# Kernel optimization log

Measured on AMD Instinct MI355X. Metric: run time of the kernel, lower is better.

Reference implementation:

```python
import jax, jax.numpy as jnp
import numpy as np


def setup_inputs() -> dict:
    key = jax.random.key(0)
    ks = jax.random.split(key, 8)
    B, C, H, W = 4, 256, 56, 56
    Cq = C // 8
    s = 0.05  # small init scale for conv weights, like kaiming-ish for 1x1 convs
    return {
        "x": jax.random.normal(ks[0], (B, C, H, W), jnp.float32),
        "Wq": jax.random.normal(ks[1], (Cq, C), jnp.float32) * s,
        "bq": jax.random.normal(ks[2], (Cq,), jnp.float32) * s,
        "Wk": jax.random.normal(ks[3], (Cq, C), jnp.float32) * s,
        "bk": jax.random.normal(ks[4], (Cq,), jnp.float32) * s,
        "Wv": jax.random.normal(ks[5], (C, C), jnp.float32) * s,
        "bv": jax.random.normal(ks[6], (C,), jnp.float32) * s,
        "gamma": jax.random.normal(ks[7], (1,), jnp.float32),
    }


def reference(x, Wq, bq, Wk, bk, Wv, bv, gamma):
    B, C, H, W = x.shape
    N = H * W
    xf = x.reshape(B, C, N)  # flatten spatial

    # 1x1 convs == channel matmuls
    q = jnp.einsum('oc,bcn->bon', Wq, xf) + bq[None, :, None]   # [B,Cq,N]
    k = jnp.einsum('oc,bcn->bon', Wk, xf) + bk[None, :, None]   # [B,Cq,N]
    v = jnp.einsum('oc,bcn->bon', Wv, xf) + bv[None, :, None]   # [B,C,N]

    # lipschitz_norm from weights: u=||Q||_F, v=max row-norm of K^T, w=max row-norm of V^T
    u = jnp.linalg.norm(Wq)
    vn = jnp.max(jnp.linalg.norm(Wk.T, axis=1))
    wn = jnp.max(jnp.linalg.norm(Wv.T, axis=1))
    norm_value = jnp.maximum(u * vn, u * wn)  # maximum(u*v, v*u, u*w)

    # energy[b,i,j] = <q[:,i], k[:,j]>, scaled by custom Lipschitz norm
    energy = jnp.einsum('bci,bcj->bij', q, k) / norm_value      # [B,N,N]
    attention = jax.nn.softmax(energy, axis=-1)

    # out[b,c,i] = sum_j v[b,c,j] * attention[b,i,j]
    out = jnp.einsum('bcj,bij->bci', v, attention).reshape(B, C, H, W)

    # lipschitz_bound: exp(sqrt(3)) * sqrt(N/C) + 2*sqrt(6)
    bound = np.float32(np.exp(np.sqrt(3.0)) * np.sqrt(N / C) + 2.0 * np.sqrt(6.0))
    out = out / bound

    return gamma * out + x
```

## Files before the change

### kernel.cpp

```cpp
#include <hip/hip_runtime.h>

#define N_SP 3136
#define C_CH 256
#define CQ   32
#define NB   4
#define JT   64
#define NJT  49
#define QT   64
#define INV_BOUND 0.04051569f
#define LOG2E 1.44269504f

typedef __attribute__((ext_vector_type(8))) short bf16x8;
typedef __attribute__((ext_vector_type(4))) float f32x4;
typedef __attribute__((ext_vector_type(2))) long long l64x2;
typedef unsigned short u16;
typedef unsigned int   u32;
typedef unsigned char  u8;
typedef long long      l64;

#define MFMA16(a,b,c) __builtin_amdgcn_mfma_f32_16x16x32_bf16(a,b,c,0,0,0)
#define MFMA8(a,b,c)  __builtin_amdgcn_mfma_f32_16x16x32_bf8_fp8(a,b,c,0,0,0)

__device__ __forceinline__ u16 f2b(float f) {
    u32 u = __builtin_bit_cast(u32, f);
    u += 0x7fffu + ((u >> 16) & 1u);
    return (u16)(u >> 16);
}
__device__ __forceinline__ u8 f2fp8(float f) {
    return (u8)(__builtin_amdgcn_cvt_pk_fp8_f32(f, f, 0, false) & 0xff);
}
__device__ __forceinline__ void dma16(const void* g, void* l) {
    __builtin_amdgcn_global_load_lds((const __attribute__((address_space(1))) u32*)g,
                                     (__attribute__((address_space(3))) u32*)l, 16, 0, 0);
}
__device__ __forceinline__ void dma4(const void* g, void* l) {
    __builtin_amdgcn_global_load_lds((const __attribute__((address_space(1))) u32*)g,
                                     (__attribute__((address_space(3))) u32*)l, 4, 0, 0);
}

__global__ __launch_bounds__(256) void stage1_kernel(
    const float* __restrict__ x, const float* __restrict__ Wq,
    const float* __restrict__ Wk, const float* __restrict__ Wv,
    u8* __restrict__ xT, u8* __restrict__ Wqb, u8* __restrict__ Wkb,
    u8* __restrict__ Wvb, float* __restrict__ scale_out,
    float* __restrict__ kmax)
{
    __shared__ float smem[64 * 65];
    const int t = threadIdx.x;
    const int bid = blockIdx.x;

    if (bid < 784) {
        float (*tile)[65] = (float(*)[65])smem;
        const int ct = bid & 3, nt = (bid >> 2) % 49, b = bid / 196;
        const int c0 = ct * 64, n0 = nt * 64;
        const int cc = t >> 4, nn4 = (t & 15) * 4;
        #pragma unroll
        for (int k = 0; k < 4; ++k) {
            int cl = cc + k * 16;
            float4 v = *(const float4*)(x + (size_t)(b * C_CH + c0 + cl) * N_SP + n0 + nn4);
            tile[cl][nn4] = v.x; tile[cl][nn4 + 1] = v.y;
            tile[cl][nn4 + 2] = v.z; tile[cl][nn4 + 3] = v.w;
        }
        __syncthreads();
        const int c4 = (t & 15) * 4, nn = t >> 4;
        #pragma unroll
        for (int k = 0; k < 4; ++k) {
            int nl = nn + k * 16;
            ushort4 o;
            o.x = f2b(tile[c4 + 0][nl]); o.y = f2b(tile[c4 + 1][nl]);
            o.z = f2b(tile[c4 + 2][nl]); o.w = f2b(tile[c4 + 3][nl]);
            const int off = ((c0 + c4) * 2) ^ ((nl & 15) << 5);
            *(ushort4*)(xT + (size_t)(b * N_SP + n0 + nl) * 512 + off) = o;
        }
    } else if (bid < 864) {
        int idx = (bid - 784) * 256 + t;
        const float* src; u8* dst; int off;
        if (idx < 2048)      { src = Wq; dst = Wqb; off = idx; }
        else if (idx < 4096) { src = Wk; dst = Wkb; off = idx - 2048; }
        else                 { src = Wv; dst = Wvb; off = idx - 4096; }
        float4 v = *(const float4*)(src + off * 4);
        ushort4 o; o.x = f2b(v.x); o.y = f2b(v.y); o.z = f2b(v.z); o.w = f2b(v.w);
        const int row = off >> 6, inner = (off & 63) * 8;
        *(ushort4*)(dst + row * 512 + (inner ^ ((row & 15) << 5))) = o;
    } else {
        if (t < NB) kmax[t] = 0.f;
        float* red = smem;
        float u2 = 0.f;
        for (int i = t; i < CQ * C_CH; i += 256) { float w = Wq[i]; u2 += w * w; }
        red[t] = u2; __syncthreads();
        #pragma unroll
        for (int s = 128; s > 0; s >>= 1) { if (t < s) red[t] += red[t + s]; __syncthreads(); }
        float u2t = red[0]; __syncthreads();
        float vn2 = 0.f;
        for (int o = 0; o < CQ; ++o)   { float w = Wk[o * C_CH + t]; vn2 += w * w; }
        float wn2 = 0.f;
        for (int o = 0; o < C_CH; ++o) { float w = Wv[o * C_CH + t]; wn2 += w * w; }
        red[t] = fmaxf(vn2, wn2); __syncthreads();
        #pragma unroll
        for (int s = 128; s > 0; s >>= 1) { if (t < s) red[t] = fmaxf(red[t], red[t + s]); __syncthreads(); }
        if (t == 0) scale_out[0] = 1.0f / (sqrtf(u2t) * sqrtf(red[0]));
    }
}

__global__ __launch_bounds__(256) void qkv_mfma(
    const u8* __restrict__ xT, const u8* __restrict__ Wqb,
    const u8* __restrict__ Wkb, const u8* __restrict__ Wvb,
    const float* __restrict__ bq, const float* __restrict__ bk,
    const float* __restrict__ bv, const float* __restrict__ scale_p,
    u16* __restrict__ qT, u8* __restrict__ Kg, u8* __restrict__ Vg,
    float* __restrict__ qnorm, float* __restrict__ kmax)
{
    __shared__ __align__(16) u8 xTl[32768];
    __shared__ __align__(16) u8 Wl[32768];

    const int t = threadIdx.x;
    const int split = blockIdx.x / 196, tile = blockIdx.x % 196;
    const int b = tile / 49, nt = tile % 49;
    const int w = t >> 6, lane = t & 63, li = t & 15, g = (t >> 4) & 3;
    const int n = nt * 64 + w * 16 + li;
    const int r0 = (split - 1) * 64;
    const f32x4 zero = {0.f, 0.f, 0.f, 0.f};

    {
        const u8* xsrc = xT + (size_t)(b * N_SP + nt * 64) * 512;
        #pragma unroll
        for (int i = 0; i < 8; ++i)
            dma16(xsrc + w * 8192 + i * 1024 + lane * 16, xTl + w * 8192 + i * 1024);
        if (split == 0) {
            #pragma unroll
            for (int i = 0; i < 4; ++i)
                dma16(Wqb + w * 4096 + i * 1024 + lane * 16, Wl + w * 4096 + i * 1024);
            #pragma unroll
            for (int i = 0; i < 4; ++i)
                dma16(Wkb + w * 4096 + i * 1024 + lane * 16, Wl + 16384 + w * 4096 + i * 1024);
        } else {
            const u8* wsrc = Wvb + (size_t)r0 * 512;
            #pragma unroll
            for (int i = 0; i < 8; ++i)
                dma16(wsrc + w * 8192 + i * 1024 + lane * 16, Wl + w * 8192 + i * 1024);
        }
    }
    asm volatile("s_waitcnt vmcnt(0)" ::: "memory");
    __syncthreads();

    const int swz = li << 5;
    bf16x8 xf[8];
    #pragma unroll
    for (int ks = 0; ks < 8; ++ks)
        xf[ks] = *(const bf16x8*)(xTl + (w * 16 + li) * 512 + ((ks * 64 + 16 * g) ^ swz));

    if (split == 0) {
        f32x4 aq0 = zero, aq1 = zero, ak0 = zero, ak1 = zero;
        #pragma unroll
        for (int ks = 0; ks < 8; ++ks) {
            const int o = (ks * 64 + 16 * g) ^ swz;
            bf16x8 w0 = *(const bf16x8*)(Wl + li * 512 + o);
            bf16x8 w1 = *(const bf16x8*)(Wl + (16 + li) * 512 + o);
            bf16x8 w2 = *(const bf16x8*)(Wl + 16384 + li * 512 + o);
            bf16x8 w3 = *(const bf16x8*)(Wl + 16384 + (16 + li) * 512 + o);
            aq0 = MFMA16(w0, xf[ks], aq0);
            aq1 = MFMA16(w1, xf[ks], aq1);
            ak0 = MFMA16(w2, xf[ks], ak0);
            ak1 = MFMA16(w3, xf[ks], ak1);
        }
        const float scf = scale_p[0] * LOG2E;
        f32x4 bq0 = *(const f32x4*)(bq + 4 * g);
        f32x4 bq1 = *(const f32x4*)(bq + 16 + 4 * g);
        f32x4 bk0 = *(const f32x4*)(bk + 4 * g);
        f32x4 bk1 = *(const f32x4*)(bk + 16 + 4 * g);
        float qn2 = 0.f, kn2 = 0.f;
        ushort4 s0, s1;
        #pragma unroll
        for (int r = 0; r < 4; ++r) {
            float q0 = (aq0[r] + bq0[r]) * scf;
            float q1 = (aq1[r] + bq1[r]) * scf;
            qn2 += q0 * q0 + q1 * q1;
            ((u16*)&s0)[r] = f2b(q0); ((u16*)&s1)[r] = f2b(q1);
        }
        *(ushort4*)(qT + (size_t)(b * N_SP + n) * CQ + 4 * g)      = s0;
        *(ushort4*)(qT + (size_t)(b * N_SP + n) * CQ + 16 + 4 * g) = s1;
        #pragma unroll
        for (int r = 0; r < 4; ++r) {
            float k0 = ak0[r] + bk0[r];
            float k1 = ak1[r] + bk1[r];
            kn2 += k0 * k0 + k1 * k1;
            ((u16*)&s0)[r] = f2b(k0); ((u16*)&s1)[r] = f2b(k1);
        }
        u8* krow = Kg + ((size_t)b * N_SP + n) * 64;
        const int swn = ((n >> 1) & 3) << 4;
        *(ushort4*)(krow + ((8 * g) ^ swn))      = s0;
        *(ushort4*)(krow + ((32 + 8 * g) ^ swn)) = s1;

        qn2 += __shfl_xor(qn2, 16); qn2 += __shfl_xor(qn2, 32);
        kn2 += __shfl_xor(kn2, 16); kn2 += __shfl_xor(kn2, 32);
        if (g == 0) qnorm[b * N_SP + n] = sqrtf(qn2);
        float kn = sqrtf(kn2);
        #pragma unroll
        for (int d = 1; d < 16; d <<= 1) kn = fmaxf(kn, __shfl_xor(kn, d));
        if ((t & 63) == 0) atomicMax((int*)(kmax + b), __float_as_int(kn));
    } else {
        f32x4 a[4] = {zero, zero, zero, zero};
        #pragma unroll
        for (int ks = 0; ks < 8; ++ks) {
            const int o = (ks * 64 + 16 * g) ^ swz;
            #pragma unroll
            for (int fr = 0; fr < 4; ++fr) {
                bf16x8 wf = *(const bf16x8*)(Wl + (fr * 16 + li) * 512 + o);
                a[fr] = MFMA16(wf, xf[ks], a[fr]);
            }
        }
        const int jj = w * 16 + li;
        const int p = ((jj >> 5) & 1) * 8 + ((jj >> 3) & 3) * 16 + (jj & 7);
        u8* vtile = Vg + (size_t)(b * NJT + nt) * 16384;
        #pragma unroll
        for (int fr = 0; fr < 4; ++fr) {
            f32x4 bb = *(const f32x4*)(bv + r0 + fr * 16 + 4 * g);
            #pragma unroll
            for (int r = 0; r < 4; ++r) {
                const int c = r0 + fr * 16 + 4 * g + r;
                vtile[c * 64 + (p ^ (((c >> 1) & 3) << 4))] = f2fp8(a[fr][r] + bb[r]);
            }
        }
    }
}

__global__ __launch_bounds__(512) void attn_mfma(
    const u16* __restrict__ qT, const u8* __restrict__ Kg,
    const u8* __restrict__ Vg, const float* __restrict__ x,
    const float* __restrict__ gamma_p, const float* __restrict__ qnorm,
    const float* __restrict__ kmax, float* __restrict__ out)
{
    __shared__ __align__(16) u8 smem[86016];
    u8* const Vl = smem;
    u8* const Kl = smem + 65536;
    u8* const Pl = smem + 81920;

    const int t = threadIdx.x;
    const int w = t >> 6, li = t & 15, g = (t >> 4) & 3;
    const int jh = w & 3, qh = w >> 2;
    const int cw = w * 32;
    const int swz = ((li >> 1) & 3) << 4;

    const int b  = blockIdx.x / NJT;
    const int i0 = (blockIdx.x % NJT) * QT;

    const u16* qTb = qT + (size_t)b * N_SP * CQ;
    const u8*  Kbb = Kg + (size_t)b * N_SP * 64;
    const u8*  Vbb = Vg + (size_t)b * NJT * 16384;
    const float kmb = kmax[b];
    const f32x4 zero = {0.f, 0.f, 0.f, 0.f};

    const int qA = 2 * qh, qB = 2 * qh + 1;
    const bf16x8 qfA = *(const bf16x8*)(qTb + (size_t)(i0 + qA * 16 + li) * CQ + 8 * g);
    const bf16x8 qfB = *(const bf16x8*)(qTb + (size_t)(i0 + qB * 16 + li) * CQ + 8 * g);
    const float mrA = qnorm[b * N_SP + i0 + qA * 16 + li] * kmb;
    const float mrB = qnorm[b * N_SP + i0 + qB * 16 + li] * kmb;

    f32x4 acc[4][2];
    #pragma unroll
    for (int qq = 0; qq < 4; ++qq) { acc[qq][0] = zero; acc[qq][1] = zero; }
    float lsA = 0.f, lsB = 0.f;

    #define ISSUE(jt_, s_) do {                                               \
        const u8* vsrc_ = Vbb + (size_t)(jt_) * 16384;                        \
        const u8* ksrc_ = Kbb + (size_t)(jt_) * 4096;                         \
        _Pragma("unroll")                                                     \
        for (int i_ = 0; i_ < 2; ++i_)                                        \
            dma16(vsrc_ + i_ * 8192 + t * 16,                                 \
                  Vl + (s_) * 16384 + i_ * 8192 + w * 1024);                  \
        _Pragma("unroll")                                                     \
        for (int i_ = 0; i_ < 2; ++i_)                                        \
            dma4(ksrc_ + i_ * 2048 + t * 4,                                   \
                 Kl + (s_) * 4096 + i_ * 2048 + w * 256);                     \
    } while (0)

    ISSUE(0, 0);
    ISSUE(1, 1);
    ISSUE(2, 2);

    const int p0 = ((jh >> 1) & 1) * 8 + ((jh * 2 + (g >> 1)) & 3) * 16 + 4 * (g & 1);

    for (int it = 0; it < NJT; ++it) {
        const int cur = it & 3;
        asm volatile("s_waitcnt vmcnt(8) lgkmcnt(0)" ::: "memory");
        __builtin_amdgcn_s_barrier();
        asm volatile("" ::: "memory");

        {
            int jn = it + 3; if (jn > NJT - 1) jn = NJT - 1;
            ISSUE(jn, (cur + 3) & 3);
        }

        const u8* Kc = Kl + cur * 4096;
        bf16x8 kf = *(const bf16x8*)(Kc + (jh * 16 + li) * 64 + ((16 * g) ^ swz));
        f32x4 sA = MFMA16(kf, qfA, zero);
        f32x4 sB = MFMA16(kf, qfB, zero);
        {
            float a0 = exp2f(sA[0] - mrA), a1 = exp2f(sA[1] - mrA);
            float a2 = exp2f(sA[2] - mrA), a3 = exp2f(sA[3] - mrA);
            lsA += (a0 + a1) + (a2 + a3);
            int pk = __builtin_amdgcn_cvt_pk_bf8_f32(a0, a1, 0, false);
            pk = __builtin_amdgcn_cvt_pk_bf8_f32(a2, a3, pk, true);
            *(u32*)(Pl + (qA * 16 + li) * 64 + (p0 ^ swz)) = (u32)pk;
            float b0 = exp2f(sB[0] - mrB), b1 = exp2f(sB[1] - mrB);
            float b2 = exp2f(sB[2] - mrB), b3 = exp2f(sB[3] - mrB);
            lsB += (b0 + b1) + (b2 + b3);
            pk = __builtin_amdgcn_cvt_pk_bf8_f32(b0, b1, 0, false);
            pk = __builtin_amdgcn_cvt_pk_bf8_f32(b2, b3, pk, true);
            *(u32*)(Pl + (qB * 16 + li) * 64 + (p0 ^ swz)) = (u32)pk;
        }
        asm volatile("s_waitcnt lgkmcnt(0)" ::: "memory");
        __builtin_amdgcn_s_barrier();
        asm volatile("" ::: "memory");

        const u8* Vc = Vl + cur * 16384;
        __builtin_amdgcn_s_setprio(1);
        l64x2 pa0 = *(const l64x2*)(Pl + (0 * 16 + li) * 64 + ((16 * g) ^ swz));
        l64x2 pa1 = *(const l64x2*)(Pl + (1 * 16 + li) * 64 + ((16 * g) ^ swz));
        l64x2 pa2 = *(const l64x2*)(Pl + (2 * 16 + li) * 64 + ((16 * g) ^ swz));
        l64x2 pa3 = *(const l64x2*)(Pl + (3 * 16 + li) * 64 + ((16 * g) ^ swz));
        l64x2 v0  = *(const l64x2*)(Vc + (cw + li) * 64 + ((16 * g) ^ swz));
        l64x2 v1  = *(const l64x2*)(Vc + (cw + 16 + li) * 64 + ((16 * g) ^ swz));
        acc[0][0] = MFMA8(pa0[0], v0[0], acc[0][0]);
        acc[0][1] = MFMA8(pa0[0], v1[0], acc[0][1]);
        acc[1][0] = MFMA8(pa1[0], v0[0], acc[1][0]);
        acc[1][1] = MFMA8(pa1[0], v1[0], acc[1][1]);
        acc[2][0] = MFMA8(pa2[0], v0[0], acc[2][0]);
        acc[2][1] = MFMA8(pa2[0], v1[0], acc[2][1]);
        acc[3][0] = MFMA8(pa3[0], v0[0], acc[3][0]);
        acc[3][1] = MFMA8(pa3[0], v1[0], acc[3][1]);
        acc[0][0] = MFMA8(pa0[1], v0[1], acc[0][0]);
        acc[0][1] = MFMA8(pa0[1], v1[1], acc[0][1]);
        acc[1][0] = MFMA8(pa1[1], v0[1], acc[1][0]);
        acc[1][1] = MFMA8(pa1[1], v1[1], acc[1][1]);
        acc[2][0] = MFMA8(pa2[1], v0[1], acc[2][0]);
        acc[2][1] = MFMA8(pa2[1], v1[1], acc[2][1]);
        acc[3][0] = MFMA8(pa3[1], v0[1], acc[3][0]);
        acc[3][1] = MFMA8(pa3[1], v1[1], acc[3][1]);
        __builtin_amdgcn_s_setprio(0);
    }
    #undef ISSUE

    lsA += __shfl_xor(lsA, 16); lsA += __shfl_xor(lsA, 32);
    lsB += __shfl_xor(lsB, 16); lsB += __shfl_xor(lsB, 32);
    __syncthreads();
    float* red       = (float*)Pl;
    float* red_final = (float*)(Pl + 1024);
    if ((t & 63) < 16) {
        red[w * 32 + li]      = lsA;
        red[w * 32 + 16 + li] = lsB;
    }
    __syncthreads();
    if (t < 64) {
        const int h = t >> 4, l2 = t & 15;
        float s = 0.f;
        #pragma unroll
        for (int jw = 0; jw < 4; ++jw)
            s += red[((h >> 1) * 4 + jw) * 32 + (h & 1) * 16 + l2];
        red_final[t] = s;
    }
    __syncthreads();

    const float gsc = gamma_p[0] * INV_BOUND;
    #pragma unroll
    for (int qq = 0; qq < 4; ++qq) {
        f32x4 lsv = *(const f32x4*)(red_final + qq * 16 + 4 * g);
        f32x4 rinv;
        #pragma unroll
        for (int r = 0; r < 4; ++r) rinv[r] = gsc / lsv[r];
        #pragma unroll
        for (int cf = 0; cf < 2; ++cf) {
            const int c = cw + cf * 16 + li;
            const size_t base = ((size_t)b * C_CH + c) * N_SP + i0 + qq * 16 + 4 * g;
            float4 xv = *(const float4*)(x + base);
            float4 o;
            o.x = acc[qq][cf][0] * rinv[0] + xv.x;
            o.y = acc[qq][cf][1] * rinv[1] + xv.y;
            o.z = acc[qq][cf][2] * rinv[2] + xv.z;
            o.w = acc[qq][cf][3] * rinv[3] + xv.w;
            *(float4*)(out + base) = o;
        }
    }
}

extern "C" void kernel_launch(void* const* d_in, const int* in_sizes, int n_in,
                              void* d_out, int out_size, void* d_ws, size_t ws_size,
                              hipStream_t stream)
{
    const float* x  = (const float*)d_in[0];
    const float* Wq = (const float*)d_in[1];
    const float* bq = (const float*)d_in[2];
    const float* Wk = (const float*)d_in[3];
    const float* bk = (const float*)d_in[4];
    const float* Wv = (const float*)d_in[5];
    const float* bv = (const float*)d_in[6];
    const float* gm = (const float*)d_in[7];
    float* out = (float*)d_out;
    float* ws  = (float*)d_ws;

    float* scale = ws;
    float* kmax  = ws + 4;
    float* qnorm = ws + 8;
    u8* Wqb = (u8*)(ws + 8 + NB * N_SP);
    u8* Wkb = Wqb + 32 * 512;
    u8* Wvb = Wkb + 32 * 512;
    u8* xT  = Wvb + 256 * 512;
    u16* qT = (u16*)(xT + (size_t)NB * N_SP * 512);
    u8* Kg  = (u8*)(qT + (size_t)NB * N_SP * CQ);
    u8* Vg  = Kg + (size_t)NB * N_SP * 64;

    stage1_kernel<<<865, 256, 0, stream>>>(x, Wq, Wk, Wv, xT, Wqb, Wkb, Wvb, scale, kmax);
    qkv_mfma<<<980, 256, 0, stream>>>(xT, Wqb, Wkb, Wvb, bq, bk, bv, scale, qT, Kg, Vg, qnorm, kmax);
    attn_mfma<<<NB * NJT, 512, 0, stream>>>(qT, Kg, Vg, x, gm, qnorm, kmax, out);
}
```

Before: 87.92 us.

## Split attention key range across two blocks with larger query tiles and combine pass

Doubles the query tile to 128 rows and splits the 49 key tiles into two halves handled by separate blocks, giving 200 blocks instead of 196. Each block writes its unnormalized bf16 numerator and row sums to the workspace, and a new combine kernel adds the two halves, normalizes, scales by gamma and adds the residual. The aim is to reuse each streamed K/V tile across more query rows, halving K/V traffic per query, while keeping the grid filled through the key split. The cost is an extra kernel launch, a partial-result round-trip through memory, bf16 rounding of the partial numerators, and more accumulator registers, which may lower occupancy.

```diff
diff --git a/kernel.cpp b/kernel.cpp
--- a/kernel.cpp
+++ b/kernel.cpp
@@ -6,7 +6,9 @@
 #define NB   4
 #define JT   64
 #define NJT  49
-#define QT   64
+#define QT   128
+#define NQT  25
+#define JSPL 2
 #define INV_BOUND 0.04051569f
 #define LOG2E 1.44269504f
 
@@ -25,6 +27,9 @@
     u32 u = __builtin_bit_cast(u32, f);
     u += 0x7fffu + ((u >> 16) & 1u);
     return (u16)(u >> 16);
+}
+__device__ __forceinline__ float b2f(u16 v) {
+    return __builtin_bit_cast(float, (u32)v << 16);
 }
 __device__ __forceinline__ u8 f2fp8(float f) {
     return (u8)(__builtin_amdgcn_cvt_pk_fp8_f32(f, f, 0, false) & 0xff);
@@ -226,11 +231,11 @@
 
 __global__ __launch_bounds__(512) void attn_mfma(
     const u16* __restrict__ qT, const u8* __restrict__ Kg,
-    const u8* __restrict__ Vg, const float* __restrict__ x,
-    const float* __restrict__ gamma_p, const float* __restrict__ qnorm,
-    const float* __restrict__ kmax, float* __restrict__ out)
+    const u8* __restrict__ Vg, const float* __restrict__ qnorm,
+    const float* __restrict__ kmax, u16* __restrict__ numP,
+    float* __restrict__ lsP)
 {
-    __shared__ __align__(16) u8 smem[86016];
+    __shared__ __align__(16) u8 smem[88064];
     u8* const Vl = smem;
     u8* const Kl = smem + 65536;
     u8* const Pl = smem + 81920;
@@ -241,8 +246,12 @@
     const int cw = w * 32;
     const int swz = ((li >> 1) & 3) << 4;
 
-    const int b  = blockIdx.x / NJT;
-    const int i0 = (blockIdx.x % NJT) * QT;
+    const int bid = blockIdx.x;
+    const int b = bid / 50, rem = bid % 50;
+    const int qt = rem >> 1, js = rem & 1;
+    const int i0 = qt * QT;
+    const int jbeg = js ? 25 : 0, jend = js ? 49 : 25;
+    const int nIter = jend - jbeg;
 
     const u16* qTb = qT + (size_t)b * N_SP * CQ;
     const u8*  Kbb = Kg + (size_t)b * N_SP * 64;
@@ -250,16 +259,19 @@
     const float kmb = kmax[b];
     const f32x4 zero = {0.f, 0.f, 0.f, 0.f};
 
-    const int qA = 2 * qh, qB = 2 * qh + 1;
-    const bf16x8 qfA = *(const bf16x8*)(qTb + (size_t)(i0 + qA * 16 + li) * CQ + 8 * g);
-    const bf16x8 qfB = *(const bf16x8*)(qTb + (size_t)(i0 + qB * 16 + li) * CQ + 8 * g);
-    const float mrA = qnorm[b * N_SP + i0 + qA * 16 + li] * kmb;
-    const float mrB = qnorm[b * N_SP + i0 + qB * 16 + li] * kmb;
-
-    f32x4 acc[4][2];
+    bf16x8 qf[4]; float mr[4];
     #pragma unroll
-    for (int qq = 0; qq < 4; ++qq) { acc[qq][0] = zero; acc[qq][1] = zero; }
-    float lsA = 0.f, lsB = 0.f;
+    for (int f = 0; f < 4; ++f) {
+        int qr = i0 + (qh * 4 + f) * 16 + li;
+        qr = qr < N_SP ? qr : N_SP - 1;
+        qf[f] = *(const bf16x8*)(qTb + (size_t)qr * CQ + 8 * g);
+        mr[f] = qnorm[b * N_SP + qr] * kmb;
+    }
+
+    f32x4 acc[8][2];
+    #pragma unroll
+    for (int qq = 0; qq < 8; ++qq) { acc[qq][0] = zero; acc[qq][1] = zero; }
+    float ls4[4] = {0.f, 0.f, 0.f, 0.f};
 
     #define ISSUE(jt_, s_) do {                                               \
         const u8* vsrc_ = Vbb + (size_t)(jt_) * 16384;                        \
@@ -274,40 +286,35 @@
                  Kl + (s_) * 4096 + i_ * 2048 + w * 256);                     \
     } while (0)
 
-    ISSUE(0, 0);
-    ISSUE(1, 1);
-    ISSUE(2, 2);
+    ISSUE(jbeg, 0);
+    ISSUE(jbeg + 1, 1);
+    ISSUE(jbeg + 2, 2);
 
     const int p0 = ((jh >> 1) & 1) * 8 + ((jh * 2 + (g >> 1)) & 3) * 16 + 4 * (g & 1);
 
-    for (int it = 0; it < NJT; ++it) {
-        const int cur = it & 3;
+    for (int ii = 0; ii < nIter; ++ii) {
+        const int it = jbeg + ii;
+        const int cur = ii & 3;
         asm volatile("s_waitcnt vmcnt(8) lgkmcnt(0)" ::: "memory");
         __builtin_amdgcn_s_barrier();
         asm volatile("" ::: "memory");
 
         {
-            int jn = it + 3; if (jn > NJT - 1) jn = NJT - 1;
+            int jn = it + 3; if (jn > jend - 1) jn = jend - 1;
             ISSUE(jn, (cur + 3) & 3);
         }
 
         const u8* Kc = Kl + cur * 4096;
         bf16x8 kf = *(const bf16x8*)(Kc + (jh * 16 + li) * 64 + ((16 * g) ^ swz));
-        f32x4 sA = MFMA16(kf, qfA, zero);
-        f32x4 sB = MFMA16(kf, qfB, zero);
-        {
-            float a0 = exp2f(sA[0] - mrA), a1 = exp2f(sA[1] - mrA);
-            float a2 = exp2f(sA[2] - mrA), a3 = exp2f(sA[3] - mrA);
-            lsA += (a0 + a1) + (a2 + a3);
+        #pragma unroll
+        for (int f = 0; f < 4; ++f) {
+            f32x4 s = MFMA16(kf, qf[f], zero);
+            float a0 = exp2f(s[0] - mr[f]), a1 = exp2f(s[1] - mr[f]);
+            float a2 = exp2f(s[2] - mr[f]), a3 = exp2f(s[3] - mr[f]);
+            ls4[f] += (a0 + a1) + (a2 + a3);
             int pk = __builtin_amdgcn_cvt_pk_bf8_f32(a0, a1, 0, false);
             pk = __builtin_amdgcn_cvt_pk_bf8_f32(a2, a3, pk, true);
-            *(u32*)(Pl + (qA * 16 + li) * 64 + (p0 ^ swz)) = (u32)pk;
-            float b0 = exp2f(sB[0] - mrB), b1 = exp2f(sB[1] - mrB);
-            float b2 = exp2f(sB[2] - mrB), b3 = exp2f(sB[3] - mrB);
-            lsB += (b0 + b1) + (b2 + b3);
-            pk = __builtin_amdgcn_cvt_pk_bf8_f32(b0, b1, 0, false);
-            pk = __builtin_amdgcn_cvt_pk_bf8_f32(b2, b3, pk, true);
-            *(u32*)(Pl + (qB * 16 + li) * 64 + (p0 ^ swz)) = (u32)pk;
+            *(u32*)(Pl + ((qh * 4 + f) * 16 + li) * 64 + (p0 ^ swz)) = (u32)pk;
         }
         asm volatile("s_waitcnt lgkmcnt(0)" ::: "memory");
         __builtin_amdgcn_s_barrier();
@@ -315,71 +322,82 @@
 
         const u8* Vc = Vl + cur * 16384;
         __builtin_amdgcn_s_setprio(1);
-        l64x2 pa0 = *(const l64x2*)(Pl + (0 * 16 + li) * 64 + ((16 * g) ^ swz));
-        l64x2 pa1 = *(const l64x2*)(Pl + (1 * 16 + li) * 64 + ((16 * g) ^ swz));
-        l64x2 pa2 = *(const l64x2*)(Pl + (2 * 16 + li) * 64 + ((16 * g) ^ swz));
-        l64x2 pa3 = *(const l64x2*)(Pl + (3 * 16 + li) * 64 + ((16 * g) ^ swz));
-        l64x2 v0  = *(const l64x2*)(Vc + (cw + li) * 64 + ((16 * g) ^ swz));
-        l64x2 v1  = *(const l64x2*)(Vc + (cw + 16 + li) * 64 + ((16 * g) ^ swz));
-        acc[0][0] = MFMA8(pa0[0], v0[0], acc[0][0]);
-        acc[0][1] = MFMA8(pa0[0], v1[0], acc[0][1]);
-        acc[1][0] = MFMA8(pa1[0], v0[0], acc[1][0]);
-        acc[1][1] = MFMA8(pa1[0], v1[0], acc[1][1]);
-        acc[2][0] = MFMA8(pa2[0], v0[0], acc[2][0]);
-        acc[2][1] = MFMA8(pa2[0], v1[0], acc[2][1]);
-        acc[3][0] = MFMA8(pa3[0], v0[0], acc[3][0]);
-        acc[3][1] = MFMA8(pa3[0], v1[0], acc[3][1]);
-        acc[0][0] = MFMA8(pa0[1], v0[1], acc[0][0]);
-        acc[0][1] = MFMA8(pa0[1], v1[1], acc[0][1]);
-        acc[1][0] = MFMA8(pa1[1], v0[1], acc[1][0]);
-        acc[1][1] = MFMA8(pa1[1], v1[1], acc[1][1]);
-        acc[2][0] = MFMA8(pa2[1], v0[1], acc[2][0]);
-        acc[2][1] = MFMA8(pa2[1], v1[1], acc[2][1]);
-        acc[3][0] = MFMA8(pa3[1], v0[1], acc[3][0]);
-        acc[3][1] = MFMA8(pa3[1], v1[1], acc[3][1]);
+        l64x2 v0 = *(const l64x2*)(Vc + (cw + li) * 64 + ((16 * g) ^ swz));
+        l64x2 v1 = *(const l64x2*)(Vc + (cw + 16 + li) * 64 + ((16 * g) ^ swz));
+        #pragma unroll
+        for (int qq = 0; qq < 8; ++qq) {
+            l64x2 pa = *(const l64x2*)(Pl + (qq * 16 + li) * 64 + ((16 * g) ^ swz));
+            acc[qq][0] = MFMA8(pa[0], v0[0], acc[qq][0]);
+            acc[qq][1] = MFMA8(pa[0], v1[0], acc[qq][1]);
+            acc[qq][0] = MFMA8(pa[1], v0[1], acc[qq][0]);
+            acc[qq][1] = MFMA8(pa[1], v1[1], acc[qq][1]);
+        }
         __builtin_amdgcn_s_setprio(0);
     }
     #undef ISSUE
 
-    lsA += __shfl_xor(lsA, 16); lsA += __shfl_xor(lsA, 32);
-    lsB += __shfl_xor(lsB, 16); lsB += __shfl_xor(lsB, 32);
+    #pragma unroll
+    for (int f = 0; f < 4; ++f) {
+        ls4[f] += __shfl_xor(ls4[f], 16);
+        ls4[f] += __shfl_xor(ls4[f], 32);
+    }
     __syncthreads();
-    float* red       = (float*)Pl;
-    float* red_final = (float*)(Pl + 1024);
+    float* red = (float*)Pl;
     if ((t & 63) < 16) {
-        red[w * 32 + li]      = lsA;
-        red[w * 32 + 16 + li] = lsB;
+        #pragma unroll
+        for (int f = 0; f < 4; ++f) red[w * 64 + f * 16 + li] = ls4[f];
     }
     __syncthreads();
-    if (t < 64) {
-        const int h = t >> 4, l2 = t & 15;
-        float s = 0.f;
-        #pragma unroll
-        for (int jw = 0; jw < 4; ++jw)
-            s += red[((h >> 1) * 4 + jw) * 32 + (h & 1) * 16 + l2];
-        red_final[t] = s;
-    }
-    __syncthreads();
-
-    const float gsc = gamma_p[0] * INV_BOUND;
+    if (t < QT) {
+        const int qh2 = t >> 6, rowin = t & 63;
+        float s = red[(qh2 * 4 + 0) * 64 + rowin] + red[(qh2 * 4 + 1) * 64 + rowin]
+                + red[(qh2 * 4 + 2) * 64 + rowin] + red[(qh2 * 4 + 3) * 64 + rowin];
+        lsP[(size_t)bid * QT + t] = s;
+    }
+
+    u16* np = numP + (size_t)bid * QT * C_CH;
     #pragma unroll
-    for (int qq = 0; qq < 4; ++qq) {
-        f32x4 lsv = *(const f32x4*)(red_final + qq * 16 + 4 * g);
-        f32x4 rinv;
-        #pragma unroll
-        for (int r = 0; r < 4; ++r) rinv[r] = gsc / lsv[r];
+    for (int qq = 0; qq < 8; ++qq) {
         #pragma unroll
         for (int cf = 0; cf < 2; ++cf) {
             const int c = cw + cf * 16 + li;
-            const size_t base = ((size_t)b * C_CH + c) * N_SP + i0 + qq * 16 + 4 * g;
-            float4 xv = *(const float4*)(x + base);
-            float4 o;
-            o.x = acc[qq][cf][0] * rinv[0] + xv.x;
-            o.y = acc[qq][cf][1] * rinv[1] + xv.y;
-            o.z = acc[qq][cf][2] * rinv[2] + xv.z;
-            o.w = acc[qq][cf][3] * rinv[3] + xv.w;
-            *(float4*)(out + base) = o;
-        }
+            ushort4 o;
+            o.x = f2b(acc[qq][cf][0]); o.y = f2b(acc[qq][cf][1]);
+            o.z = f2b(acc[qq][cf][2]); o.w = f2b(acc[qq][cf][3]);
+            *(ushort4*)(np + c * QT + qq * 16 + 4 * g) = o;
+        }
+    }
+}
+
+__global__ __launch_bounds__(256) void attn_combine(
+    const u16* __restrict__ numP, const float* __restrict__ lsP,
+    const float* __restrict__ x, const float* __restrict__ gamma_p,
+    float* __restrict__ out)
+{
+    const int bid = blockIdx.x;
+    const int b = bid / 100, rem = bid % 100;
+    const int qt = rem >> 2, qq4 = rem & 3;
+    const int i0 = qt * QT;
+    if (i0 + qq4 * 32 >= N_SP) return;
+
+    const int t = threadIdx.x;
+    const int q32 = t & 31, cg = t >> 5;
+    const int qloc = qq4 * 32 + q32;
+    const int qglob = i0 + qloc;
+
+    const size_t blk0 = ((size_t)b * NQT + qt) * 2;
+    const float lsf = lsP[blk0 * QT + qloc] + lsP[(blk0 + 1) * QT + qloc];
+    const float rinv = gamma_p[0] * INV_BOUND / lsf;
+
+    const u16* np0 = numP + blk0 * QT * C_CH;
+    const u16* np1 = np0 + QT * C_CH;
+
+    #pragma unroll 8
+    for (int cc = 0; cc < 32; ++cc) {
+        const int c = cg * 32 + cc;
+        float num = b2f(np0[c * QT + qloc]) + b2f(np1[c * QT + qloc]);
+        const size_t base = ((size_t)b * C_CH + c) * N_SP + qglob;
+        out[base] = num * rinv + x[base];
     }
 }
 
@@ -408,8 +426,11 @@
     u16* qT = (u16*)(xT + (size_t)NB * N_SP * 512);
     u8* Kg  = (u8*)(qT + (size_t)NB * N_SP * CQ);
     u8* Vg  = Kg + (size_t)NB * N_SP * 64;
+    u16* numP = (u16*)(Vg + (size_t)NB * NJT * 16384);
+    float* lsP = (float*)(numP + (size_t)200 * QT * C_CH);
 
     stage1_kernel<<<865, 256, 0, stream>>>(x, Wq, Wk, Wv, xT, Wqb, Wkb, Wvb, scale, kmax);
     qkv_mfma<<<980, 256, 0, stream>>>(xT, Wqb, Wkb, Wvb, bq, bk, bv, scale, qT, Kg, Vg, qnorm, kmax);
-    attn_mfma<<<NB * NJT, 512, 0, stream>>>(qT, Kg, Vg, x, gm, qnorm, kmax, out);
-}
+    attn_mfma<<<200, 512, 0, stream>>>(qT, Kg, Vg, qnorm, kmax, numP, lsP);
+    attn_combine<<<400, 256, 0, stream>>>(numP, lsP, x, gm, out);
+}
```

New measurement: 93.84 us. +6.7%, slower.

## Split attention key range across two blocks and add combine kernel

Applied to the files above, without the earlier changes.

The attention kernel now splits the 49 key tiles into two halves, so there are twice as many blocks (392 vs 196) to better fill the GPU's compute units. Each block writes a bf16 partial numerator and partial row sums to workspace, and a new combine kernel adds them, normalizes, and applies the gamma/residual. The pipeline drops from 4 to 3 LDS stages to cut shared memory per block, with launch bounds hinting higher occupancy. The trade-off is an extra kernel launch, extra global traffic for the partials, and bf16 rounding of the partial numerators.

```diff
diff --git a/kernel.cpp b/kernel.cpp
--- a/kernel.cpp
+++ b/kernel.cpp
@@ -7,6 +7,7 @@
 #define JT   64
 #define NJT  49
 #define QT   64
+#define JSPL 2
 #define INV_BOUND 0.04051569f
 #define LOG2E 1.44269504f
 
@@ -25,6 +26,9 @@
     u32 u = __builtin_bit_cast(u32, f);
     u += 0x7fffu + ((u >> 16) & 1u);
     return (u16)(u >> 16);
+}
+__device__ __forceinline__ float b2f(u16 v) {
+    return __builtin_bit_cast(float, (u32)v << 16);
 }
 __device__ __forceinline__ u8 f2fp8(float f) {
     return (u8)(__builtin_amdgcn_cvt_pk_fp8_f32(f, f, 0, false) & 0xff);
@@ -224,16 +228,16 @@
     }
 }
 
-__global__ __launch_bounds__(512) void attn_mfma(
+__global__ __launch_bounds__(512, 4) void attn_mfma(
     const u16* __restrict__ qT, const u8* __restrict__ Kg,
-    const u8* __restrict__ Vg, const float* __restrict__ x,
-    const float* __restrict__ gamma_p, const float* __restrict__ qnorm,
-    const float* __restrict__ kmax, float* __restrict__ out)
+    const u8* __restrict__ Vg, const float* __restrict__ qnorm,
+    const float* __restrict__ kmax, u16* __restrict__ numP,
+    float* __restrict__ lsP)
 {
-    __shared__ __align__(16) u8 smem[86016];
+    __shared__ __align__(16) u8 smem[65536];
     u8* const Vl = smem;
-    u8* const Kl = smem + 65536;
-    u8* const Pl = smem + 81920;
+    u8* const Kl = smem + 49152;
+    u8* const Pl = smem + 61440;
 
     const int t = threadIdx.x;
     const int w = t >> 6, li = t & 15, g = (t >> 4) & 3;
@@ -241,8 +245,12 @@
     const int cw = w * 32;
     const int swz = ((li >> 1) & 3) << 4;
 
-    const int b  = blockIdx.x / NJT;
-    const int i0 = (blockIdx.x % NJT) * QT;
+    const int bid = blockIdx.x;
+    const int b = bid / 98, rem = bid % 98;
+    const int qt = rem >> 1, js = rem & 1;
+    const int i0 = qt * QT;
+    const int jbeg = js ? 25 : 0, jend = js ? 49 : 25;
+    const int nIter = jend - jbeg;
 
     const u16* qTb = qT + (size_t)b * N_SP * CQ;
     const u8*  Kbb = Kg + (size_t)b * N_SP * 64;
@@ -274,21 +282,22 @@
                  Kl + (s_) * 4096 + i_ * 2048 + w * 256);                     \
     } while (0)
 
-    ISSUE(0, 0);
-    ISSUE(1, 1);
-    ISSUE(2, 2);
+    ISSUE(jbeg, 0);
+    ISSUE(jbeg + 1, 1);
 
     const int p0 = ((jh >> 1) & 1) * 8 + ((jh * 2 + (g >> 1)) & 3) * 16 + 4 * (g & 1);
 
-    for (int it = 0; it < NJT; ++it) {
-        const int cur = it & 3;
-        asm volatile("s_waitcnt vmcnt(8) lgkmcnt(0)" ::: "memory");
+    int cur = 0;
+    for (int ii = 0; ii < nIter; ++ii) {
+        const int it = jbeg + ii;
+        asm volatile("s_waitcnt vmcnt(4) lgkmcnt(0)" ::: "memory");
         __builtin_amdgcn_s_barrier();
         asm volatile("" ::: "memory");
 
         {
-            int jn = it + 3; if (jn > NJT - 1) jn = NJT - 1;
-            ISSUE(jn, (cur + 3) & 3);
+            int jn = it + 2; if (jn > jend - 1) jn = jend - 1;
+            int s2 = cur + 2; if (s2 >= 3) s2 -= 3;
+            ISSUE(jn, s2);
         }
 
         const u8* Kc = Kl + cur * 4096;
@@ -338,48 +347,69 @@
         acc[3][0] = MFMA8(pa3[1], v0[1], acc[3][0]);
         acc[3][1] = MFMA8(pa3[1], v1[1], acc[3][1]);
         __builtin_amdgcn_s_setprio(0);
+
+        ++cur; if (cur == 3) cur = 0;
     }
     #undef ISSUE
 
     lsA += __shfl_xor(lsA, 16); lsA += __shfl_xor(lsA, 32);
     lsB += __shfl_xor(lsB, 16); lsB += __shfl_xor(lsB, 32);
     __syncthreads();
-    float* red       = (float*)Pl;
-    float* red_final = (float*)(Pl + 1024);
+    float* red = (float*)Pl;
     if ((t & 63) < 16) {
         red[w * 32 + li]      = lsA;
         red[w * 32 + 16 + li] = lsB;
     }
     __syncthreads();
-    if (t < 64) {
+    if (t < QT) {
         const int h = t >> 4, l2 = t & 15;
         float s = 0.f;
         #pragma unroll
         for (int jw = 0; jw < 4; ++jw)
             s += red[((h >> 1) * 4 + jw) * 32 + (h & 1) * 16 + l2];
-        red_final[t] = s;
-    }
-    __syncthreads();
-
-    const float gsc = gamma_p[0] * INV_BOUND;
+        lsP[(size_t)bid * QT + t] = s;
+    }
+
+    u16* np = numP + (size_t)bid * QT * C_CH;
     #pragma unroll
     for (int qq = 0; qq < 4; ++qq) {
-        f32x4 lsv = *(const f32x4*)(red_final + qq * 16 + 4 * g);
-        f32x4 rinv;
-        #pragma unroll
-        for (int r = 0; r < 4; ++r) rinv[r] = gsc / lsv[r];
         #pragma unroll
         for (int cf = 0; cf < 2; ++cf) {
             const int c = cw + cf * 16 + li;
-            const size_t base = ((size_t)b * C_CH + c) * N_SP + i0 + qq * 16 + 4 * g;
-            float4 xv = *(const float4*)(x + base);
-            float4 o;
-            o.x = acc[qq][cf][0] * rinv[0] + xv.x;
-            o.y = acc[qq][cf][1] * rinv[1] + xv.y;
-            o.z = acc[qq][cf][2] * rinv[2] + xv.z;
-            o.w = acc[qq][cf][3] * rinv[3] + xv.w;
-            *(float4*)(out + base) = o;
-        }
+            ushort4 o;
+            o.x = f2b(acc[qq][cf][0]); o.y = f2b(acc[qq][cf][1]);
+            o.z = f2b(acc[qq][cf][2]); o.w = f2b(acc[qq][cf][3]);
+            *(ushort4*)(np + c * QT + qq * 16 + 4 * g) = o;
+        }
+    }
+}
+
+__global__ __launch_bounds__(256) void attn_combine(
+    const u16* __restrict__ numP, const float* __restrict__ lsP,
+    const float* __restrict__ x, const float* __restrict__ gamma_p,
+    float* __restrict__ out)
+{
+    const int bid = blockIdx.x;
+    const int b = bid / 49, qt = bid % 49;
+    const int i0 = qt * QT;
+
+    const int t = threadIdx.x;
+    const int qloc = t & 63, cg = t >> 6;
+    const int qglob = i0 + qloc;
+
+    const size_t blk0 = ((size_t)b * 49 + qt) * 2;
+    const float lsf = lsP[blk0 * QT + qloc] + lsP[(blk0 + 1) * QT + qloc];
+    const float rinv = gamma_p[0] * INV_BOUND / lsf;
+
+    const u16* np0 = numP + blk0 * QT * C_CH;
+    const u16* np1 = np0 + QT * C_CH;
+
+    #pragma unroll 8
+    for (int cc = 0; cc < 64; ++cc) {
+        const int c = cg * 64 + cc;
+        float num = b2f(np0[c * QT + qloc]) + b2f(np1[c * QT + qloc]);
+        const size_t base = ((size_t)b * C_CH + c) * N_SP + qglob;
+        out[base] = num * rinv + x[base];
     }
 }
 
@@ -408,8 +438,11 @@
     u16* qT = (u16*)(xT + (size_t)NB * N_SP * 512);
     u8* Kg  = (u8*)(qT + (size_t)NB * N_SP * CQ);
     u8* Vg  = Kg + (size_t)NB * N_SP * 64;
+    u16* numP = (u16*)(Vg + (size_t)NB * NJT * 16384);
+    float* lsP = (float*)(numP + (size_t)392 * QT * C_CH);
 
     stage1_kernel<<<865, 256, 0, stream>>>(x, Wq, Wk, Wv, xT, Wqb, Wkb, Wvb, scale, kmax);
     qkv_mfma<<<980, 256, 0, stream>>>(xT, Wqb, Wkb, Wvb, bq, bk, bv, scale, qT, Kg, Vg, qnorm, kmax);
-    attn_mfma<<<NB * NJT, 512, 0, stream>>>(qT, Kg, Vg, x, gm, qnorm, kmax, out);
-}
+    attn_mfma<<<NB * NJT * JSPL, 512, 0, stream>>>(qT, Kg, Vg, qnorm, kmax, numP, lsP);
+    attn_combine<<<NB * NJT, 256, 0, stream>>>(numP, lsP, x, gm, out);
+}
```

Result: slower. 90.75 us (+3.2%).
